# Performance work log

Measured on AMD Instinct MI355X. Metric: run time of the kernel, lower is better.

## Reference

```python
import jax, jax.numpy as jnp
import numpy as np

N = 100_000   # nodes
E = 3_200_000 # directed edges (avg degree 32)
D = 256       # feature dim (in_channels)
K = 2         # k of k-MIS


def _propagate_min(min_rank, row, col, n, k):
    # k iterations of scatter_min along edges (row -> col), keeping current value
    for _ in range(k):
        neigh = jax.ops.segment_min(min_rank[row], col, num_segments=n)
        min_rank = jnp.minimum(min_rank, neigh)
    return min_rank


def maximal_k_independent_set(row, col, rank, n, k):
    # Luby-style greedy k-MIS: repeatedly add nodes whose rank is minimal in their
    # k-hop in-neighbourhood, then mark (cover) the k-hop neighbourhood of the MIS.
    def dilate(mask):
        for _ in range(k):
            neigh = jax.ops.segment_max(mask[row].astype(jnp.int32), col, num_segments=n)
            mask = mask | (neigh > 0)
        return mask

    def cond(state):
        _, mask, _ = state
        return ~jnp.all(mask)

    def body(state):
        mis, mask, min_rank = state
        min_rank = _propagate_min(min_rank, row, col, n, k)
        mis = mis | (rank == min_rank)
        mask = dilate(mis)
        min_rank = jnp.where(mask, n, rank)  # covered nodes get rank 'infinity' (= n)
        return mis, mask, min_rank

    z = jnp.zeros((n,), dtype=bool)
    mis, _, _ = jax.lax.while_loop(cond, body, (z, z, rank))
    return mis


def cluster_k_mis(mis, row, col, rank, n, k):
    # min_rank = n everywhere except MIS nodes get their rank; propagate min k hops;
    # cluster id = index of the unique MIS rank each node ends up attached to.
    min_rank = jnp.where(mis, rank, n)
    min_rank = _propagate_min(min_rank, row, col, n, k)
    _, clusters = jnp.unique(min_rank, return_inverse=True)
    return clusters.reshape(-1).astype(jnp.int32)


def setup_inputs():
    key = jax.random.key(0)
    k1, k2, k3 = jax.random.split(key, 3)
    x = jax.random.normal(k1, (N, D), dtype=jnp.float32)
    edge_index = jax.random.randint(k2, (2, E), 0, N, dtype=jnp.int32)
    edge_attr = jax.random.normal(k3, (E,), dtype=jnp.float32)
    return {"x": x, "edge_index": edge_index, "edge_attr": edge_attr}


def reference(x, edge_index, edge_attr):
    n = x.shape[0]
    row, col = edge_index[0], edge_index[1]
    # scorer=None -> score = arange(n); greedy ordering of arange -> rank = arange(n)
    rank = jnp.arange(n, dtype=jnp.int32)

    mis = maximal_k_independent_set(row, col, rank, n, K)
    cluster = cluster_k_mis(mis, row, col, rank, n, K)
    c = int(mis.sum())  # number of clusters (MIS size)

    # --- pooled adjacency: coalesce duplicate (cluster[row], cluster[col]) with sum ---
    cl_np = np.asarray(cluster).astype(np.int64)
    r = cl_np[np.asarray(row)]
    cc = cl_np[np.asarray(col)]
    keys = r * np.int64(c) + cc
    uniq, inv = np.unique(keys, return_inverse=True)
    val = jax.ops.segment_sum(edge_attr, jnp.asarray(inv.astype(np.int32)),
                              num_segments=int(uniq.shape[0]))
    new_row = (uniq // c).astype(np.int32)
    new_col = (uniq % c).astype(np.int32)
    keep = np.nonzero(new_row != new_col)[0]  # remove_self_loops=True
    pooled_edge_index = jnp.stack([jnp.asarray(new_row[keep]), jnp.asarray(new_col[keep])])
    pooled_edge_attr = val[jnp.asarray(keep)]

    # --- pooled node features: reduce_x='sum' (adaptive=False, so no score scaling) ---
    x_pooled = jax.ops.segment_sum(x, cluster, num_segments=c)
    return x_pooled, pooled_edge_index, pooled_edge_attr
```

## Files before the change

kernel.cpp:

```cpp
#include <hip/hip_runtime.h>
#include <cmath>
#include <cstdint>

#define NT 256
#define EG0 1024
#define EG1 256
#define MAX_ROUND 16
#define SCAN_T 32
#define SCAN_IPB (NT*SCAN_T)
#define SENT 0x80000000u


__device__ __forceinline__ int block_append(int* cursor, bool pred, int* s_w){
  int wid  = threadIdx.x >> 6;
  int lane = threadIdx.x & 63;
  unsigned long long m = __ballot(pred);
  int cnt = __popcll(m);
  if(lane==0) s_w[wid]=cnt;
  __syncthreads();
  if(threadIdx.x==0){
    int t0=s_w[0], t1=s_w[1], t2=s_w[2], t3=s_w[3];
    int tot=t0+t1+t2+t3;
    int base = tot ? atomicAdd(cursor, tot) : 0;
    s_w[0]=base; s_w[1]=base+t0; s_w[2]=base+t0+t1; s_w[3]=base+t0+t1+t2;
  }
  __syncthreads();
  int pos = s_w[wid] + __popcll(m & ((1ull<<lane)-1ull));
  __syncthreads();
  return pos;
}


__global__ void k_init(int* a, int* b, int n){
  int v = blockIdx.x*NT + threadIdx.x;
  if(v<n){ a[v]=v; b[v]=v; }
}

__global__ void k_fill_dense(float* dense, long M){
  long stride = (long)gridDim.x*NT;
  for(long i = (long)blockIdx.x*NT + threadIdx.x; i<M; i+=stride)
    ((unsigned int*)dense)[i] = SENT;
}


__global__ void k_hop0(int* b, const int* __restrict__ row,
                       const int* __restrict__ col, int E){
  int stride = gridDim.x*NT;
  for(int e = blockIdx.x*NT + threadIdx.x; e<E; e+=stride){
    int s = row[e];
    if(s < b[col[e]]) atomicMin(&b[col[e]], s);
  }
}

__global__ void k_hop0f(int* a, const int* b, const int* __restrict__ row,
                        const int* __restrict__ col, int n, int E){
  int stride = gridDim.x*NT;
  int total = n + E;
  for(int i = blockIdx.x*NT + threadIdx.x; i<total; i+=stride){
    if(i<n){
      if(b[i] < a[i]) atomicMin(&a[i], b[i]);
    } else {
      int e = i-n;
      int s = b[row[e]];
      if(s < a[col[e]]) atomicMin(&a[col[e]], s);
    }
  }
}

__global__ void k_dil0(const int* a, int* d2, int* cover, const int* __restrict__ row,
                       const int* __restrict__ col, int E, int ep){
  int stride = gridDim.x*NT;
  for(int e = blockIdx.x*NT + threadIdx.x; e<E; e+=stride){
    int r = row[e];
    if(a[r]==r){
      int cc = col[e];
      d2[r]=ep;  cover[r]=1;
      d2[cc]=ep; cover[cc]=1;
    }
  }
}

__global__ void k_dil20(const int* a, const int* d2, int* cover, const int* __restrict__ row,
                        const int* __restrict__ col, int E, int ep){
  int stride = gridDim.x*NT;
  for(int e = blockIdx.x*NT + threadIdx.x; e<E; e+=stride){
    int r = row[e];
    if((d2[r]==ep || a[r]==r) && !cover[col[e]]) cover[col[e]]=1;
  }
}

__global__ void k_fincomp0(int* a, int* b, int* mis, int* cover, int n,
                           const int* __restrict__ row, const int* __restrict__ col, int E,
                           int2* Ld, int* lcnt1, int* U1, int* rcnt0){
  __shared__ int s_w[4];
  long nth = (long)gridDim.x*NT;
  for(long base = (long)blockIdx.x*NT; base < n; base += nth){
    int v = (int)base + threadIdx.x;
    bool unc = false;
    if(v<n){
      int nw = (a[v]==v);
      if(nw){ mis[v]=1; if(!cover[v]) cover[v]=1; }
      int cov = cover[v] | nw;
      int val = cov ? n : v;
      a[v]=val; b[v]=val;
      unc = !cov;
    }
    int pos = block_append(rcnt0, unc, s_w);
    if(unc) U1[pos]=v;
  }
  for(long base = (long)blockIdx.x*NT; base < E; base += nth){
    int e = (int)base + threadIdx.x;
    bool keep=false; int2 ed;
    if(e<E){
      ed = make_int2(row[e], col[e]);
      keep = (!cover[ed.x]) || (!cover[ed.y]);
    }
    int pos = block_append(lcnt1, keep, s_w);
    if(keep) Ld[pos]=ed;
  }
}


__global__ void k_hop1(int* b, const int* a, const int2* L, const int* pE,
                       const int* gate){
  if(*gate==0) return;
  int E = *pE;
  int stride = gridDim.x*NT;
  for(int e = blockIdx.x*NT + threadIdx.x; e<E; e+=stride){
    int2 ed = L[e];
    int s = a[ed.x];
    if(s < b[ed.y]) atomicMin(&b[ed.y], s);
  }
}

__global__ void k_hop1f(int* a, const int* b, const int2* L, const int* pE,
                        const int* U, const int* pU, const int* gate){
  if(*gate==0) return;
  int E = *pE, un = *pU;
  int total = un + E;
  int stride = gridDim.x*NT;
  for(int i = blockIdx.x*NT + threadIdx.x; i<total; i+=stride){
    if(i<un){
      int u = U[i];
      if(b[u] < a[u]) atomicMin(&a[u], b[u]);
    } else {
      int2 ed = L[i-un];
      int s = b[ed.x];
      if(s < a[ed.y]) atomicMin(&a[ed.y], s);
    }
  }
}

__global__ void k_dil11(const int* a, int* d2, int* cover, int* mis, const int2* L,
                        const int* pE, const int* U, const int* pU, const int* gate, int ep){
  if(*gate==0) return;
  int E = *pE, un = *pU;
  int total = un + E;
  int stride = gridDim.x*NT;
  for(int i = blockIdx.x*NT + threadIdx.x; i<total; i+=stride){
    if(i<un){
      int u = U[i];
      if(a[u]==u){ mis[u]=1; cover[u]=1; d2[u]=ep; }
    } else {
      int2 ed = L[i-un];
      if(a[ed.x]==ed.x){ d2[ed.x]=ep; cover[ed.x]=1; d2[ed.y]=ep; cover[ed.y]=1; }
    }
  }
}

__global__ void k_dil21(const int* a, const int* d2, int* cover, const int2* L,
                        const int* pE, const int* gate, int ep){
  if(*gate==0) return;
  int E = *pE;
  int stride = gridDim.x*NT;
  for(int e = blockIdx.x*NT + threadIdx.x; e<E; e+=stride){
    int2 ed = L[e];
    if((d2[ed.x]==ep || a[ed.x]==ed.x) && !cover[ed.y]) cover[ed.y]=1;
  }
}

__global__ void k_fincomp1(int* a, int* b, const int* cover, int n,
                           const int2* Ls, const int* pE, int2* Ld, int* lcntD,
                           const int* Us, const int* pU, int* Ud, int* rcntD,
                           const int* gate){
  if(*gate==0) return;
  __shared__ int s_w[4];
  int E = *pE, un = *pU;
  long nth = (long)gridDim.x*NT;
  for(long base = (long)blockIdx.x*NT; base < un; base += nth){
    int i = (int)base + threadIdx.x;
    bool unc=false; int u=0;
    if(i<un){ u = Us[i]; unc = !cover[u]; }
    int pos = block_append(rcntD, unc, s_w);
    if(unc) Ud[pos]=u;
  }
  for(long base = (long)blockIdx.x*NT; base < E; base += nth){
    int e = (int)base + threadIdx.x;
    bool keep=false; int2 ed;
    if(e<E){
      ed = Ls[e];
      int vx = cover[ed.x] ? n : ed.x;  a[ed.x]=vx; b[ed.x]=vx;
      int vy = cover[ed.y] ? n : ed.y;  a[ed.y]=vy; b[ed.y]=vy;
      keep = (!cover[ed.x]) || (!cover[ed.y]);
    }
    int pos = block_append(lcntD, keep, s_w);
    if(keep) Ld[pos]=ed;
  }
}


__global__ void k_cluster_init(const int* mis, int* a, int* b, int n){
  int v = blockIdx.x*NT + threadIdx.x;
  if(v<n){ int m = mis[v] ? v : n; a[v]=m; b[v]=m; }
}

__global__ void k_chop1(int* b, const int* a, const int* __restrict__ row,
                        const int* __restrict__ col, int n, int E){
  int stride = gridDim.x*NT;
  for(int e = blockIdx.x*NT + threadIdx.x; e<E; e+=stride){
    int s = a[row[e]];
    if(s < n && s < b[col[e]]) atomicMin(&b[col[e]], s);
  }
}

__global__ void k_chop2f(int* a, const int* b, const int* __restrict__ row,
                         const int* __restrict__ col, int n, int E){
  int stride = gridDim.x*NT;
  int total = n + E;
  for(int i = blockIdx.x*NT + threadIdx.x; i<total; i+=stride){
    if(i<n){
      if(b[i] < a[i]) atomicMin(&a[i], b[i]);
    } else {
      int e = i-n;
      int s = b[row[e]];
      if(s < n && s < a[col[e]]) atomicMin(&a[col[e]], s);
    }
  }
}

__global__ void k_mark(const int* mr, const int* mis, int* present, int* cmis, int n){
  int v = blockIdx.x*NT + threadIdx.x;
  int m = 0;
  if(v<n){
    int r = mr[v];
    if(r<n) present[r]=1;
    m = mis[v];
  }
  __shared__ int sh[NT];
  sh[threadIdx.x]=m; __syncthreads();
  for(int off=NT/2; off>0; off>>=1){
    if(threadIdx.x<off) sh[threadIdx.x]+=sh[threadIdx.x+off];
    __syncthreads();
  }
  if(threadIdx.x==0 && sh[0]) atomicAdd(cmis, sh[0]);
}


__global__ void k_scan1(const int* A, int M, int* bsum){
  int t = threadIdx.x;
  long base = (long)blockIdx.x*SCAN_IPB + (long)t*SCAN_T;
  int s = 0;
  #pragma unroll
  for(int j=0;j<SCAN_T;j++){ long i=base+j; if(i<M) s += A[i]; }
  __shared__ int sh[NT];
  sh[t]=s; __syncthreads();
  for(int off=NT/2; off>0; off>>=1){ if(t<off) sh[t]+=sh[t+off]; __syncthreads(); }
  if(t==0) bsum[blockIdx.x]=sh[0];
}

__global__ void k_scan2(const int* bsum, int* bscan, int B, int* totalOut){
  __shared__ int sh[NT];
  int t = threadIdx.x;
  int carry = 0;
  for(int base=0; base<B; base+=NT){
    int i = base+t;
    int v = (i<B) ? bsum[i] : 0;
    sh[t]=v; __syncthreads();
    for(int off=1; off<NT; off<<=1){
      int x=0; if(t>=off) x=sh[t-off];
      __syncthreads();
      sh[t]+=x; __syncthreads();
    }
    int incl = sh[t];
    if(i<B) bscan[i] = carry + incl - v;
    carry += sh[NT-1];
    __syncthreads();
  }
  if(t==0 && totalOut) *totalOut = carry;
}

__global__ void k_scan3(const int* A, int M, const int* bscan, int* pref){
  int t = threadIdx.x;
  long base = (long)blockIdx.x*SCAN_IPB + (long)t*SCAN_T;
  int s = 0;
  #pragma unroll
  for(int j=0;j<SCAN_T;j++){ long i=base+j; if(i<M) s += A[i]; }
  __shared__ int sh[NT];
  sh[t]=s; __syncthreads();
  for(int off=1; off<NT; off<<=1){
    int x=0; if(t>=off) x=sh[t-off];
    __syncthreads();
    sh[t]+=x; __syncthreads();
  }
  int run = bscan[blockIdx.x] + (sh[t]-s);
  for(int j=0;j<SCAN_T;j++){
    long i=base+j;
    if(i<M){ pref[i]=run; run += A[i]; }
  }
}


__global__ void k_assign(const int* mr, const int* pref, int* cl, int* ccount, int n){
  int v = blockIdx.x*NT + threadIdx.x;
  if(v<n){
    int r = mr[v];
    int cid = (r<n) ? pref[r] : 0;
    cl[v]=cid;
    atomicAdd(&ccount[cid],1);
  }
}

__global__ void k_scatter_nodes(const int* cl, const int* cstart, int* cursor, int* nodeList, int n){
  int v = blockIdx.x*NT + threadIdx.x;
  if(v<n){
    int cid = cl[v];
    int pos = cstart[cid] + atomicAdd(&cursor[cid],1);
    nodeList[pos]=v;
  }
}

__global__ void k_pool_x(const float* __restrict__ x, const int* nodeList, const int* cstart,
                         const int* ccount, const int* scal, float* out, long out_size){
  int c = scal[0], U = scal[1];
  int t = threadIdx.x;
  for(int cid=blockIdx.x; cid<c; cid+=gridDim.x){
    float s0=0.f, s1=0.f, s2=0.f, s3=0.f;
    if(cid<U){
      int st = cstart[cid], cn = ccount[cid];
      int i=0;
      for(; i+3<cn; i+=4){
        int n0=nodeList[st+i], n1=nodeList[st+i+1], n2=nodeList[st+i+2], n3=nodeList[st+i+3];
        s0 += x[(size_t)n0*256 + t];
        s1 += x[(size_t)n1*256 + t];
        s2 += x[(size_t)n2*256 + t];
        s3 += x[(size_t)n3*256 + t];
      }
      for(; i<cn; i++) s0 += x[(size_t)nodeList[st+i]*256 + t];
      s0 += s1+s2+s3;
    }
    long idx = (long)cid*256 + t;
    if(idx < out_size) out[idx]=s0;
  }
}

__global__ void k_edge_pool(const int* __restrict__ row, const int* __restrict__ col,
                            const float* __restrict__ attr, const int* cl,
                            const int* scal, float* dense, int E, long CMsq){
  int c = scal[0];
  int stride = gridDim.x*NT;
  for(int e = blockIdx.x*NT + threadIdx.x; e<E; e+=stride){
    long key = (long)cl[row[e]]*c + cl[col[e]];
    if(key < CMsq){
      unsafeAtomicAdd(&dense[key], attr[e]);
    }
  }
}

__device__ __forceinline__ int cellp(const float* dense, long i){
  return __float_as_uint(dense[i]) != SENT;
}

__global__ void k_cscan1(const float* dense, const int* scal, int* bsum, long CMsq){
  int c = scal[0];
  long M = (long)c*c; if(M>CMsq) M=CMsq;
  int t = threadIdx.x;
  long base = (long)blockIdx.x*SCAN_IPB + (long)t*SCAN_T;
  int s = 0;
  if(base < M && c > 0){
    int r = (int)(base / c);
    int q = (int)(base - (long)r*c);
    for(int j=0;j<SCAN_T;j++){
      long i=base+j;
      if(i<M){
        if(cellp(dense,i) && r!=q) s++;
      }
      if(++q==c){ q=0; r++; }
    }
  }
  __shared__ int sh[NT];
  sh[t]=s; __syncthreads();
  for(int off=NT/2; off>0; off>>=1){ if(t<off) sh[t]+=sh[t+off]; __syncthreads(); }
  if(t==0) bsum[blockIdx.x]=sh[0];
}

__global__ void k_cemit(const float* dense, const int* scal,
                        const int* bscan, float* out, long out_size, long CMsq){
  int c = scal[0]; int P = scal[2];
  long M = (long)c*c; if(M>CMsq) M=CMsq;
  long xoff = (long)c*256;
  int t = threadIdx.x;
  long base = (long)blockIdx.x*SCAN_IPB + (long)t*SCAN_T;
  int s = 0;
  int r0=0,q0=0;
  if(base < M && c > 0){
    r0 = (int)(base / c);
    q0 = (int)(base - (long)r0*c);
    int r=r0, q=q0;
    for(int j=0;j<SCAN_T;j++){
      long i=base+j;
      if(i<M){
        if(cellp(dense,i) && r!=q) s++;
      }
      if(++q==c){ q=0; r++; }
    }
  }
  __shared__ int sh[NT];
  sh[t]=s; __syncthreads();
  for(int off=1; off<NT; off<<=1){
    int x=0; if(t>=off) x=sh[t-off];
    __syncthreads();
    sh[t]+=x; __syncthreads();
  }
  int run = bscan[blockIdx.x] + (sh[t]-s);
  if(base < M && c > 0){
    int r=r0, q=q0;
    for(int j=0;j<SCAN_T;j++){
      long i=base+j;
      if(i<M && cellp(dense,i) && r!=q){
        long o0 = xoff + run;
        long o1 = xoff + (long)P + run;
        long o2 = xoff + 2L*(long)P + run;
        if(o0<out_size) out[o0]=(float)r;
        if(o1<out_size) out[o1]=(float)q;
        if(o2<out_size) out[o2]=dense[i];
        run++;
      }
      if(++q==c){ q=0; r++; }
    }
  }
}


extern "C" void kernel_launch(void* const* d_in, const int* in_sizes, int n_in,
                              void* d_out, int out_size, void* d_ws, size_t ws_size,
                              hipStream_t stream){
  (void)n_in;
  const float* x     = (const float*)d_in[0];
  const int*   eidx  = (const int*)d_in[1];
  const float* eattr = (const float*)d_in[2];
  const int D = 256;
  int n = in_sizes[0]/D;
  int E = in_sizes[1]/2;
  const int* row = eidx;
  const int* col = eidx + E;

  char* p = (char*)d_ws;
  auto alloc = [&](size_t bytes)->char*{ char* r=p; p += (bytes+255)&~(size_t)255; return r; };
  int2* LA   = (int2*)alloc((size_t)E*8);
  int2* LB   = (int2*)alloc((size_t)E*8);
  int* a     = (int*)alloc((size_t)n*4);
  int* b     = (int*)alloc((size_t)n*4);
  int* cl    = (int*)alloc((size_t)n*4);
  int* nodeList = (int*)alloc((size_t)n*4);
  int* pref  = (int*)alloc((size_t)n*4);
  int* U1    = (int*)alloc((size_t)n*4);
  int* U2    = (int*)alloc((size_t)n*4);
  int* bsum  = (int*)alloc(4096*4);
  int* bscan = (int*)alloc(4096*4);
  char* zstart = p;
  int* mis     = (int*)alloc((size_t)n*4);
  int* cover   = (int*)alloc((size_t)n*4);
  int* d2      = (int*)alloc((size_t)n*4);
  int* present = (int*)alloc((size_t)n*4);
  int* ccount  = (int*)alloc((size_t)n*4);
  int* cursor  = (int*)alloc((size_t)n*4);
  int* rcnt    = (int*)alloc((MAX_ROUND+2)*4);
  int* lcnt    = (int*)alloc((MAX_ROUND+2)*4);
  int* scal    = (int*)alloc(64);
  size_t zbytes = (size_t)(p - zstart);

  size_t used   = (size_t)(p-(char*)d_ws);
  size_t remain = (ws_size > used+4096) ? ws_size-used-4096 : 0;
  size_t cells  = remain/4;
  long CM = (long)std::sqrt((double)cells);
  while(CM>1 && CM*CM > (long)cells) CM--;
  if(CM>4096) CM=4096;
  if(CM<1) CM=1;
  long CMsq = CM*CM;
  float* dense = (float*)alloc((size_t)CMsq*4);

  hipMemsetAsync(zstart, 0, zbytes, stream);
  k_fill_dense<<<2048,NT,0,stream>>>(dense, CMsq);

  int NB  = (n+NT-1)/NT;
  int NBs = (n+SCAN_IPB-1)/SCAN_IPB;
  int CB  = (int)((CMsq+SCAN_IPB-1)/SCAN_IPB);

  k_init    <<<NB,NT,0,stream>>>(a,b,n);
  k_hop0    <<<EG0,NT,0,stream>>>(b,row,col,E);
  k_hop0f   <<<EG0,NT,0,stream>>>(a,b,row,col,n,E);
  k_dil0    <<<EG0,NT,0,stream>>>(a,d2,cover,row,col,E,1);
  k_dil20   <<<EG0,NT,0,stream>>>(a,d2,cover,row,col,E,1);
  k_fincomp0<<<EG0,NT,0,stream>>>(a,b,mis,cover,n,row,col,E,LB,&lcnt[1],U1,&rcnt[0]);

  for(int r=1; r<MAX_ROUND; ++r){
    int2* Ls = (r&1) ? LB : LA;
    int2* Ld = (r&1) ? LA : LB;
    int*  Us = (r&1) ? U1 : U2;
    int*  Ud = (r&1) ? U2 : U1;
    int ep = r+1;
    k_hop1    <<<EG1,NT,0,stream>>>(b,a,Ls,&lcnt[r],&rcnt[r-1]);
    k_hop1f   <<<EG1,NT,0,stream>>>(a,b,Ls,&lcnt[r],Us,&rcnt[r-1],&rcnt[r-1]);
    k_dil11   <<<EG1,NT,0,stream>>>(a,d2,cover,mis,Ls,&lcnt[r],Us,&rcnt[r-1],&rcnt[r-1],ep);
    k_dil21   <<<EG1,NT,0,stream>>>(a,d2,cover,Ls,&lcnt[r],&rcnt[r-1],ep);
    k_fincomp1<<<EG1,NT,0,stream>>>(a,b,cover,n,Ls,&lcnt[r],Ld,&lcnt[r+1],
                                    Us,&rcnt[r-1],Ud,&rcnt[r],&rcnt[r-1]);
  }

  k_cluster_init<<<NB,NT,0,stream>>>(mis,a,b,n);
  k_chop1 <<<EG0,NT,0,stream>>>(b,a,row,col,n,E);
  k_chop2f<<<EG0,NT,0,stream>>>(a,b,row,col,n,E);

  k_mark <<<NB,NT,0,stream>>>(a,mis,present,scal,n);
  k_scan1<<<NBs,NT,0,stream>>>(present,n,bsum);
  k_scan2<<<1,NT,0,stream>>>(bsum,bscan,NBs,scal+1);
  k_scan3<<<NBs,NT,0,stream>>>(present,n,bscan,pref);
  k_assign<<<NB,NT,0,stream>>>(a,pref,cl,ccount,n);

  k_scan1<<<NBs,NT,0,stream>>>(ccount,n,bsum);
  k_scan2<<<1,NT,0,stream>>>(bsum,bscan,NBs,nullptr);
  k_scan3<<<NBs,NT,0,stream>>>(ccount,n,bscan,pref);
  k_scatter_nodes<<<NB,NT,0,stream>>>(cl,pref,cursor,nodeList,n);

  k_pool_x<<<1024,NT,0,stream>>>(x,nodeList,pref,ccount,scal,(float*)d_out,(long)out_size);

  k_edge_pool<<<EG0,NT,0,stream>>>(row,col,eattr,cl,scal,dense,E,CMsq);
  k_cscan1<<<CB,NT,0,stream>>>(dense,scal,bsum,CMsq);
  k_scan2 <<<1,NT,0,stream>>>(bsum,bscan,CB,scal+2);
  k_cemit <<<CB,NT,0,stream>>>(dense,scal,bscan,(float*)d_out,(long)out_size,CMsq);
}
```

Measured before the change: 1.914 ms.

## Use bitmaps for cover/dilation flags and size dense fill by cluster count

Replaces the int cover and epoch-tagged d2 arrays with 32-bit-word bitmaps, set via check-then-atomicOr and cleared at the end of each compaction kernel. This shrinks the random-access footprint of the dilation and compaction kernels so more of it can stay in cache. The dense-matrix sentinel fill now runs after the cluster count is known and fills only c*c cells instead of the whole workspace. The edge-pool grid is also doubled. Risks include atomic contention on shared bitmap words. The dil20 condition also changes: it no longer checks a[r]==r, relying on d2b having been set for those nodes.

```diff
diff --git a/kernel.cpp b/kernel.cpp
--- a/kernel.cpp
+++ b/kernel.cpp
@@ -4,12 +4,21 @@
 
 #define NT 256
 #define EG0 1024
+#define EGP 2048
 #define EG1 256
 #define MAX_ROUND 16
 #define SCAN_T 32
 #define SCAN_IPB (NT*SCAN_T)
 #define SENT 0x80000000u
 
+
+__device__ __forceinline__ int getbit(const unsigned int* bm, int v){
+  return (bm[v>>5]>>(v&31))&1u;
+}
+__device__ __forceinline__ void setbit(unsigned int* bm, int v){
+  unsigned int m = 1u<<(v&31);
+  if(!(bm[v>>5]&m)) atomicOr(&bm[v>>5], m);
+}
 
 __device__ __forceinline__ int block_append(int* cursor, bool pred, int* s_w){
   int wid  = threadIdx.x >> 6;
@@ -36,7 +45,9 @@
   if(v<n){ a[v]=v; b[v]=v; }
 }
 
-__global__ void k_fill_dense(float* dense, long M){
+__global__ void k_fill_dense(float* dense, const int* scal, long CMsq){
+  long c = scal[0];
+  long M = c*c; if(M>CMsq) M=CMsq;
   long stride = (long)gridDim.x*NT;
   for(long i = (long)blockIdx.x*NT + threadIdx.x; i<M; i+=stride)
     ((unsigned int*)dense)[i] = SENT;
@@ -67,29 +78,29 @@
   }
 }
 
-__global__ void k_dil0(const int* a, int* d2, int* cover, const int* __restrict__ row,
-                       const int* __restrict__ col, int E, int ep){
+__global__ void k_dil0(const int* a, unsigned int* d2b, unsigned int* coverb,
+                       const int* __restrict__ row, const int* __restrict__ col, int E){
   int stride = gridDim.x*NT;
   for(int e = blockIdx.x*NT + threadIdx.x; e<E; e+=stride){
     int r = row[e];
     if(a[r]==r){
       int cc = col[e];
-      d2[r]=ep;  cover[r]=1;
-      d2[cc]=ep; cover[cc]=1;
-    }
-  }
-}
-
-__global__ void k_dil20(const int* a, const int* d2, int* cover, const int* __restrict__ row,
-                        const int* __restrict__ col, int E, int ep){
-  int stride = gridDim.x*NT;
-  for(int e = blockIdx.x*NT + threadIdx.x; e<E; e+=stride){
-    int r = row[e];
-    if((d2[r]==ep || a[r]==r) && !cover[col[e]]) cover[col[e]]=1;
-  }
-}
-
-__global__ void k_fincomp0(int* a, int* b, int* mis, int* cover, int n,
+      setbit(d2b,r);  setbit(coverb,r);
+      setbit(d2b,cc); setbit(coverb,cc);
+    }
+  }
+}
+
+__global__ void k_dil20(const unsigned int* d2b, unsigned int* coverb,
+                        const int* __restrict__ row, const int* __restrict__ col, int E){
+  int stride = gridDim.x*NT;
+  for(int e = blockIdx.x*NT + threadIdx.x; e<E; e+=stride){
+    if(getbit(d2b,row[e])) setbit(coverb,col[e]);
+  }
+}
+
+__global__ void k_fincomp0(int* a, int* b, int* mis, unsigned int* coverb,
+                           unsigned int* d2b, int nwords, int n,
                            const int* __restrict__ row, const int* __restrict__ col, int E,
                            int2* Ld, int* lcnt1, int* U1, int* rcnt0){
   __shared__ int s_w[4];
@@ -99,8 +110,8 @@
     bool unc = false;
     if(v<n){
       int nw = (a[v]==v);
-      if(nw){ mis[v]=1; if(!cover[v]) cover[v]=1; }
-      int cov = cover[v] | nw;
+      int cov = getbit(coverb,v) | nw;
+      if(nw){ mis[v]=1; setbit(coverb,v); }
       int val = cov ? n : v;
       a[v]=val; b[v]=val;
       unc = !cov;
@@ -113,11 +124,13 @@
     bool keep=false; int2 ed;
     if(e<E){
       ed = make_int2(row[e], col[e]);
-      keep = (!cover[ed.x]) || (!cover[ed.y]);
+      keep = (!getbit(coverb,ed.x)) || (!getbit(coverb,ed.y));
     }
     int pos = block_append(lcnt1, keep, s_w);
     if(keep) Ld[pos]=ed;
   }
+  int stride = gridDim.x*NT;
+  for(int w = blockIdx.x*NT + threadIdx.x; w<nwords; w+=stride) d2b[w]=0;
 }
 
 
@@ -151,8 +164,9 @@
   }
 }
 
-__global__ void k_dil11(const int* a, int* d2, int* cover, int* mis, const int2* L,
-                        const int* pE, const int* U, const int* pU, const int* gate, int ep){
+__global__ void k_dil11(const int* a, unsigned int* d2b, unsigned int* coverb, int* mis,
+                        const int2* L, const int* pE, const int* U, const int* pU,
+                        const int* gate){
   if(*gate==0) return;
   int E = *pE, un = *pU;
   int total = un + E;
@@ -160,26 +174,30 @@
   for(int i = blockIdx.x*NT + threadIdx.x; i<total; i+=stride){
     if(i<un){
       int u = U[i];
-      if(a[u]==u){ mis[u]=1; cover[u]=1; d2[u]=ep; }
+      if(a[u]==u){ mis[u]=1; setbit(coverb,u); setbit(d2b,u); }
     } else {
       int2 ed = L[i-un];
-      if(a[ed.x]==ed.x){ d2[ed.x]=ep; cover[ed.x]=1; d2[ed.y]=ep; cover[ed.y]=1; }
-    }
-  }
-}
-
-__global__ void k_dil21(const int* a, const int* d2, int* cover, const int2* L,
-                        const int* pE, const int* gate, int ep){
+      if(a[ed.x]==ed.x){
+        setbit(d2b,ed.x); setbit(coverb,ed.x);
+        setbit(d2b,ed.y); setbit(coverb,ed.y);
+      }
+    }
+  }
+}
+
+__global__ void k_dil21(const unsigned int* d2b, unsigned int* coverb, const int2* L,
+                        const int* pE, const int* gate){
   if(*gate==0) return;
   int E = *pE;
   int stride = gridDim.x*NT;
   for(int e = blockIdx.x*NT + threadIdx.x; e<E; e+=stride){
     int2 ed = L[e];
-    if((d2[ed.x]==ep || a[ed.x]==ed.x) && !cover[ed.y]) cover[ed.y]=1;
-  }
-}
-
-__global__ void k_fincomp1(int* a, int* b, const int* cover, int n,
+    if(getbit(d2b,ed.x)) setbit(coverb,ed.y);
+  }
+}
+
+__global__ void k_fincomp1(int* a, int* b, const unsigned int* coverb,
+                           unsigned int* d2b, int nwords, int n,
                            const int2* Ls, const int* pE, int2* Ld, int* lcntD,
                            const int* Us, const int* pU, int* Ud, int* rcntD,
                            const int* gate){
@@ -190,7 +208,7 @@
   for(long base = (long)blockIdx.x*NT; base < un; base += nth){
     int i = (int)base + threadIdx.x;
     bool unc=false; int u=0;
-    if(i<un){ u = Us[i]; unc = !cover[u]; }
+    if(i<un){ u = Us[i]; unc = !getbit(coverb,u); }
     int pos = block_append(rcntD, unc, s_w);
     if(unc) Ud[pos]=u;
   }
@@ -199,13 +217,16 @@
     bool keep=false; int2 ed;
     if(e<E){
       ed = Ls[e];
-      int vx = cover[ed.x] ? n : ed.x;  a[ed.x]=vx; b[ed.x]=vx;
-      int vy = cover[ed.y] ? n : ed.y;  a[ed.y]=vy; b[ed.y]=vy;
-      keep = (!cover[ed.x]) || (!cover[ed.y]);
+      int cx = getbit(coverb,ed.x), cy = getbit(coverb,ed.y);
+      int vx = cx ? n : ed.x;  a[ed.x]=vx; b[ed.x]=vx;
+      int vy = cy ? n : ed.y;  a[ed.y]=vy; b[ed.y]=vy;
+      keep = (!cx) || (!cy);
     }
     int pos = block_append(lcntD, keep, s_w);
     if(keep) Ld[pos]=ed;
   }
+  int stride = gridDim.x*NT;
+  for(int w = blockIdx.x*NT + threadIdx.x; w<nwords; w+=stride) d2b[w]=0;
 }
 
 
@@ -453,6 +474,7 @@
   int E = in_sizes[1]/2;
   const int* row = eidx;
   const int* col = eidx + E;
+  int nwords = (n+31)>>5;
 
   char* p = (char*)d_ws;
   auto alloc = [&](size_t bytes)->char*{ char* r=p; p += (bytes+255)&~(size_t)255; return r; };
@@ -469,8 +491,8 @@
   int* bscan = (int*)alloc(4096*4);
   char* zstart = p;
   int* mis     = (int*)alloc((size_t)n*4);
-  int* cover   = (int*)alloc((size_t)n*4);
-  int* d2      = (int*)alloc((size_t)n*4);
+  unsigned int* coverb = (unsigned int*)alloc((size_t)nwords*4);
+  unsigned int* d2b    = (unsigned int*)alloc((size_t)nwords*4);
   int* present = (int*)alloc((size_t)n*4);
   int* ccount  = (int*)alloc((size_t)n*4);
   int* cursor  = (int*)alloc((size_t)n*4);
@@ -490,7 +512,6 @@
   float* dense = (float*)alloc((size_t)CMsq*4);
 
   hipMemsetAsync(zstart, 0, zbytes, stream);
-  k_fill_dense<<<2048,NT,0,stream>>>(dense, CMsq);
 
   int NB  = (n+NT-1)/NT;
   int NBs = (n+SCAN_IPB-1)/SCAN_IPB;
@@ -499,21 +520,20 @@
   k_init    <<<NB,NT,0,stream>>>(a,b,n);
   k_hop0    <<<EG0,NT,0,stream>>>(b,row,col,E);
   k_hop0f   <<<EG0,NT,0,stream>>>(a,b,row,col,n,E);
-  k_dil0    <<<EG0,NT,0,stream>>>(a,d2,cover,row,col,E,1);
-  k_dil20   <<<EG0,NT,0,stream>>>(a,d2,cover,row,col,E,1);
-  k_fincomp0<<<EG0,NT,0,stream>>>(a,b,mis,cover,n,row,col,E,LB,&lcnt[1],U1,&rcnt[0]);
+  k_dil0    <<<EG0,NT,0,stream>>>(a,d2b,coverb,row,col,E);
+  k_dil20   <<<EG0,NT,0,stream>>>(d2b,coverb,row,col,E);
+  k_fincomp0<<<EG0,NT,0,stream>>>(a,b,mis,coverb,d2b,nwords,n,row,col,E,LB,&lcnt[1],U1,&rcnt[0]);
 
   for(int r=1; r<MAX_ROUND; ++r){
     int2* Ls = (r&1) ? LB : LA;
     int2* Ld = (r&1) ? LA : LB;
     int*  Us = (r&1) ? U1 : U2;
     int*  Ud = (r&1) ? U2 : U1;
-    int ep = r+1;
     k_hop1    <<<EG1,NT,0,stream>>>(b,a,Ls,&lcnt[r],&rcnt[r-1]);
     k_hop1f   <<<EG1,NT,0,stream>>>(a,b,Ls,&lcnt[r],Us,&rcnt[r-1],&rcnt[r-1]);
-    k_dil11   <<<EG1,NT,0,stream>>>(a,d2,cover,mis,Ls,&lcnt[r],Us,&rcnt[r-1],&rcnt[r-1],ep);
-    k_dil21   <<<EG1,NT,0,stream>>>(a,d2,cover,Ls,&lcnt[r],&rcnt[r-1],ep);
-    k_fincomp1<<<EG1,NT,0,stream>>>(a,b,cover,n,Ls,&lcnt[r],Ld,&lcnt[r+1],
+    k_dil11   <<<EG1,NT,0,stream>>>(a,d2b,coverb,mis,Ls,&lcnt[r],Us,&rcnt[r-1],&rcnt[r-1]);
+    k_dil21   <<<EG1,NT,0,stream>>>(d2b,coverb,Ls,&lcnt[r],&rcnt[r-1]);
+    k_fincomp1<<<EG1,NT,0,stream>>>(a,b,coverb,d2b,nwords,n,Ls,&lcnt[r],Ld,&lcnt[r+1],
                                     Us,&rcnt[r-1],Ud,&rcnt[r],&rcnt[r-1]);
   }
 
@@ -527,6 +547,8 @@
   k_scan3<<<NBs,NT,0,stream>>>(present,n,bscan,pref);
   k_assign<<<NB,NT,0,stream>>>(a,pref,cl,ccount,n);
 
+  k_fill_dense<<<2048,NT,0,stream>>>(dense,scal,CMsq);
+
   k_scan1<<<NBs,NT,0,stream>>>(ccount,n,bsum);
   k_scan2<<<1,NT,0,stream>>>(bsum,bscan,NBs,nullptr);
   k_scan3<<<NBs,NT,0,stream>>>(ccount,n,bscan,pref);
@@ -534,7 +556,7 @@
 
   k_pool_x<<<1024,NT,0,stream>>>(x,nodeList,pref,ccount,scal,(float*)d_out,(long)out_size);
 
-  k_edge_pool<<<EG0,NT,0,stream>>>(row,col,eattr,cl,scal,dense,E,CMsq);
+  k_edge_pool<<<EGP,NT,0,stream>>>(row,col,eattr,cl,scal,dense,E,CMsq);
   k_cscan1<<<CB,NT,0,stream>>>(dense,scal,bsum,CMsq);
   k_scan2 <<<1,NT,0,stream>>>(bsum,bscan,CB,scal+2);
   k_cemit <<<CB,NT,0,stream>>>(dense,scal,bscan,(float*)d_out,(long)out_size,CMsq);
```

Result: slower. 2.022 ms (+5.6%).
